# Optimization experiments

Hardware: AMD Instinct MI355X
Metric: run time of the kernel (lower is better)

Reference implementation:

```python
import jax, jax.numpy as jnp
import numpy as np

EPS = 1e-5

def setup_inputs() -> dict:
    key = jax.random.key(0)
    ks = jax.random.split(key, 8)
    B, T, D, S = 8, 4096, 1024, 64
    return {
        "x": jax.random.normal(ks[0], (B, T, D), dtype=jnp.float32),
        "time_decay": jax.random.normal(ks[1], (S,), dtype=jnp.float32) * 0.1 - 0.5,
        "time_first": jax.random.normal(ks[2], (S,), dtype=jnp.float32) * 0.1,
        "W_key": jax.random.normal(ks[3], (S, D), dtype=jnp.float32) * 0.02,
        "W_value": jax.random.normal(ks[4], (S, D), dtype=jnp.float32) * 0.02,
        "W_output": jax.random.normal(ks[5], (D, S), dtype=jnp.float32) * 0.02,
        "W_shift": jax.random.normal(ks[6], (D, D), dtype=jnp.float32) * 0.02,
        "shift_gate": jnp.ones((D,), dtype=jnp.float32),
        "ln_w": jnp.ones((D,), dtype=jnp.float32),
        "ln_b": jnp.zeros((D,), dtype=jnp.float32),
    }


def _forward(x, time_decay, time_first, W_key, W_value, W_output, W_shift, shift_gate, ln_w, ln_b):
    B, T, D = x.shape
    S = time_decay.shape[0]
    # --- token shift: rotate sequence by shift_len, project, gated blend ---
    shift_len = max(1, int(T * 0.5))
    x_cat = jnp.concatenate([x[:, shift_len:], x[:, :-shift_len]], axis=1)  # (B,T,D)
    gate = jax.nn.sigmoid(shift_gate)
    x_shift = jnp.einsum('btd,ed->bte', x_cat, W_shift) * gate + x * (1.0 - gate)
    # --- layernorm (torch: biased variance, eps=1e-5) ---
    mu = jnp.mean(x_shift, axis=-1, keepdims=True)
    var = jnp.mean(jnp.square(x_shift - mu), axis=-1, keepdims=True)
    xn = (x_shift - mu) * jax.lax.rsqrt(var + EPS) * ln_w + ln_b
    # --- key/value projections and per-step wkv (fully vectorized) ---
    k = jnp.einsum('btd,sd->bts', xn, W_key)    # (B,T,S)
    v = jnp.einsum('btd,sd->bts', xn, W_value)  # (B,T,S)
    wkv = jnp.exp(-jnp.exp(time_first) * jax.nn.sigmoid(k)) * v  # (B,T,S)
    # --- linear recurrence: state = state*w + wkv_t, scanned over T ---
    w = jnp.exp(time_decay)  # (S,)
    def step(state, wkv_t):
        state = state * w + wkv_t
        return state, state
    init = jnp.zeros((B, S), dtype=x.dtype)
    last_state, states = jax.lax.scan(step, init, jnp.swapaxes(wkv, 0, 1))  # states: (T,B,S)
    states = jnp.swapaxes(states, 0, 1)  # (B,T,S)
    # --- batched output projection (applied per-step in torch; same math) ---
    output = jnp.einsum('bts,ds->btd', states, W_output)  # (B,T,D)
    return output, last_state


def reference(x, time_decay, time_first, W_key, W_value, W_output, W_shift, shift_gate, ln_w, ln_b):
    out, last_state = _forward(x, time_decay, time_first, W_key, W_value, W_output, W_shift, shift_gate, ln_w, ln_b)
    return out, jax.lax.stop_gradient(last_state)
```

## Files before the change

### kernel.cpp

```cpp
#include <hip/hip_runtime.h>
#include <stdint.h>

#define B_ 8
#define T_ 4096
#define D_ 1024
#define S_ 64
#define N_ 32768
#define OUT_ELEMS 33554432
#define NCHK 128
#define CHKL 32

typedef __attribute__((ext_vector_type(8))) short bf16x8;
typedef __attribute__((ext_vector_type(8))) unsigned short u16x8;
typedef __attribute__((ext_vector_type(4))) float f32x4;

__device__ __forceinline__ uint16_t f2bf(float f) {
    union { float f; uint32_t u; } v; v.f = f;
    uint32_t r = v.u + 0x7FFFu + ((v.u >> 16) & 1u);
    return (uint16_t)(r >> 16);
}
__device__ __forceinline__ float bf2f(uint16_t h) {
    union { uint32_t u; float f; } v; v.u = ((uint32_t)h) << 16;
    return v.f;
}

#define GLOAD_LDS16(gp, lp)                                             \
    __builtin_amdgcn_global_load_lds(                                   \
        (const __attribute__((address_space(1))) void*)(gp),            \
        (__attribute__((address_space(3))) void*)(lp), 16, 0, 0)

__global__ void cast_f32_bf16(const float* __restrict__ src,
                              uint16_t* __restrict__ dst, int n4) {
    int i = blockIdx.x * blockDim.x + threadIdx.x;
    if (i >= n4) return;
    float4 v = ((const float4*)src)[i];
    ushort4 o;
    o.x = f2bf(v.x); o.y = f2bf(v.y); o.z = f2bf(v.z); o.w = f2bf(v.w);
    ((ushort4*)dst)[i] = o;
}

__global__ __launch_bounds__(256) void k1_shift_gemm(
    const uint16_t* __restrict__ xb, const uint16_t* __restrict__ Wsb,
    const float* __restrict__ shift_gate, uint16_t* __restrict__ xs)
{
    __shared__ uint16_t As[128][64];
    __shared__ uint16_t Bs[128][64];
    const int tid = threadIdx.x;
    const int w = tid >> 6, lane = tid & 63, quad = lane >> 4, l16 = lane & 15;
    const int wm = w >> 1, wn = w & 1;
    const int m0 = blockIdx.y * 128;
    const int n0 = blockIdx.x * 128;
    const int m0x = m0 ^ 2048;

    const int srow = w * 32 + (lane >> 3);
    const int scg  = ((lane & 7) ^ (lane >> 3)) * 8;
    const uint16_t* aG = xb  + (size_t)(m0x + srow) * D_ + scg;
    const uint16_t* bG = Wsb + (size_t)(n0  + srow) * D_ + scg;

    f32x4 acc[4][4];
#pragma unroll
    for (int i = 0; i < 4; ++i)
#pragma unroll
        for (int j = 0; j < 4; ++j) acc[i][j] = (f32x4){0.f, 0.f, 0.f, 0.f};

    for (int k0 = 0; k0 < D_; k0 += 64) {
        __syncthreads();
#pragma unroll
        for (int i = 0; i < 4; ++i) {
            GLOAD_LDS16(aG + k0 + (size_t)(i * 8) * D_, &As[w * 32 + i * 8][0]);
            GLOAD_LDS16(bG + k0 + (size_t)(i * 8) * D_, &Bs[w * 32 + i * 8][0]);
        }
        __syncthreads();
#pragma unroll
        for (int ks = 0; ks < 2; ++ks) {
            bf16x8 a[4], b[4];
#pragma unroll
            for (int i = 0; i < 4; ++i) {
                int ra = wm * 64 + i * 16 + l16;
                a[i] = *(const bf16x8*)&As[ra][(((ks * 4 + quad) ^ (l16 & 7)) * 8)];
            }
#pragma unroll
            for (int j = 0; j < 4; ++j) {
                int rb = wn * 64 + j * 16 + l16;
                b[j] = *(const bf16x8*)&Bs[rb][(((ks * 4 + quad) ^ (l16 & 7)) * 8)];
            }
#pragma unroll
            for (int i = 0; i < 4; ++i)
#pragma unroll
                for (int j = 0; j < 4; ++j)
                    acc[i][j] = __builtin_amdgcn_mfma_f32_16x16x32_bf16(
                        a[i], b[j], acc[i][j], 0, 0, 0);
        }
    }

#pragma unroll
    for (int j = 0; j < 4; ++j) {
        int col = n0 + wn * 64 + j * 16 + l16;
        float g = 1.f / (1.f + __expf(-shift_gate[col]));
        float omg = 1.f - g;
#pragma unroll
        for (int i = 0; i < 4; ++i) {
            int row = m0 + wm * 64 + i * 16 + quad * 4;
#pragma unroll
            for (int r = 0; r < 4; ++r) {
                float res = acc[i][j][r] * g +
                            bf2f(xb[(size_t)(row + r) * D_ + col]) * omg;
                xs[(size_t)(row + r) * D_ + col] = f2bf(res);
            }
        }
    }
}

__global__ __launch_bounds__(256) void k2_ln(uint16_t* __restrict__ xs,
                                             const float* __restrict__ ln_w,
                                             const float* __restrict__ ln_b)
{
    const int w = threadIdx.x >> 6, lane = threadIdx.x & 63;
    const size_t row = (size_t)blockIdx.x * 4 + w;
    uint16_t* p = xs + row * D_ + lane * 16;

    u16x8 h0 = *(const u16x8*)p;
    u16x8 h1 = *(const u16x8*)(p + 8);
    float v[16];
#pragma unroll
    for (int i = 0; i < 8; ++i) { v[i] = bf2f(h0[i]); v[8 + i] = bf2f(h1[i]); }
    float s = 0.f, q = 0.f;
#pragma unroll
    for (int i = 0; i < 16; ++i) { s += v[i]; q += v[i] * v[i]; }
#pragma unroll
    for (int off = 32; off > 0; off >>= 1) {
        s += __shfl_xor(s, off);
        q += __shfl_xor(q, off);
    }
    float mu = s * (1.f / D_);
    float var = q * (1.f / D_) - mu * mu;
    float rstd = rsqrtf(var + 1e-5f);

    const float* lw = ln_w + lane * 16;
    const float* lb = ln_b + lane * 16;
    u16x8 o0, o1;
#pragma unroll
    for (int i = 0; i < 8; ++i) {
        o0[i] = f2bf((v[i] - mu) * rstd * lw[i] + lb[i]);
        o1[i] = f2bf((v[8 + i] - mu) * rstd * lw[8 + i] + lb[8 + i]);
    }
    *(u16x8*)p = o0;
    *(u16x8*)(p + 8) = o1;
}

__global__ __launch_bounds__(256) void k3_kv(
    const uint16_t* __restrict__ xn, const uint16_t* __restrict__ Wkvb,
    const float* __restrict__ time_first, float* __restrict__ wkv)
{
    __shared__ float tile[2][128][65];
    const int tid = threadIdx.x;
    const int w = tid >> 6, lane = tid & 63, quad = lane >> 4, l16 = lane & 15;
    const int wm = w >> 1, wn = w & 1;
    const int bm0 = blockIdx.x * 128;
    const int m0 = bm0 + wm * 64;

    const uint16_t* aptr[4];
    const uint16_t* bptr[4];
#pragma unroll
    for (int i = 0; i < 4; ++i) {
        aptr[i] = xn + (size_t)(m0 + i * 16 + l16) * D_ + quad * 8;
        bptr[i] = Wkvb + (size_t)(wn * 64 + i * 16 + l16) * D_ + quad * 8;
    }

    f32x4 acc[4][4];
#pragma unroll
    for (int i = 0; i < 4; ++i)
#pragma unroll
        for (int j = 0; j < 4; ++j) acc[i][j] = (f32x4){0.f, 0.f, 0.f, 0.f};

    for (int k = 0; k < D_; k += 32) {
        bf16x8 a[4], b[4];
#pragma unroll
        for (int i = 0; i < 4; ++i) a[i] = *(const bf16x8*)(aptr[i] + k);
#pragma unroll
        for (int i = 0; i < 4; ++i) b[i] = *(const bf16x8*)(bptr[i] + k);
#pragma unroll
        for (int i = 0; i < 4; ++i)
#pragma unroll
            for (int j = 0; j < 4; ++j)
                acc[i][j] = __builtin_amdgcn_mfma_f32_16x16x32_bf16(
                    a[i], b[j], acc[i][j], 0, 0, 0);
    }

#pragma unroll
    for (int i = 0; i < 4; ++i)
#pragma unroll
        for (int j = 0; j < 4; ++j)
#pragma unroll
            for (int r = 0; r < 4; ++r) {
                int rl = wm * 64 + i * 16 + quad * 4 + r;
                int cl = j * 16 + l16;
                tile[wn][rl][cl] = acc[i][j][r];
            }
    __syncthreads();

    for (int e = tid; e < 128 * 64; e += 256) {
        int rl = e >> 6, s = e & 63;
        float kk = tile[0][rl][s];
        float vv = tile[1][rl][s];
        float sig = 1.f / (1.f + __expf(-kk));
        float res = __expf(-__expf(time_first[s]) * sig) * vv;
        wkv[(size_t)(bm0 + rl) * S_ + s] = res;
    }
}

__global__ void k4a(const float* __restrict__ wkv,
                    const float* __restrict__ time_decay,
                    float* __restrict__ part)
{
    const int s = threadIdx.x;
    const int bc = blockIdx.x;
    const int b = bc >> 7, c = bc & (NCHK - 1);
    float w = expf(time_decay[s]);
    const float* src = wkv + ((size_t)b * T_ + c * CHKL) * S_ + s;
    float st = 0.f;
    for (int t = 0; t < CHKL; ++t) st = st * w + src[(size_t)t * S_];
    part[(size_t)bc * S_ + s] = st;
}
__global__ void k4b(const float* __restrict__ part,
                    const float* __restrict__ time_decay,
                    float* __restrict__ carry)
{
    const int s = threadIdx.x;
    const int b = blockIdx.x;
    float wL = expf(time_decay[s] * (float)CHKL);
    float cin = 0.f;
    for (int c = 0; c < NCHK; ++c) {
        size_t idx = ((size_t)b * NCHK + c) * S_ + s;
        carry[idx] = cin;
        cin = cin * wL + part[idx];
    }
}
__global__ void k4c(const float* __restrict__ wkv,
                    const float* __restrict__ time_decay,
                    const float* __restrict__ carry,
                    uint16_t* __restrict__ stb,
                    float* __restrict__ last_state)
{
    const int s = threadIdx.x;
    const int bc = blockIdx.x;
    const int b = bc >> 7, c = bc & (NCHK - 1);
    float w = expf(time_decay[s]);
    const float* src = wkv + ((size_t)b * T_ + c * CHKL) * S_ + s;
    uint16_t* dst = stb + ((size_t)b * T_ + c * CHKL) * S_ + s;
    float st = carry[(size_t)bc * S_ + s];
    for (int t = 0; t < CHKL; ++t) {
        st = st * w + src[(size_t)t * S_];
        dst[(size_t)t * S_] = f2bf(st);
    }
    if (c == NCHK - 1) last_state[b * S_ + s] = st;
}

__global__ __launch_bounds__(256) void k5_out(
    const uint16_t* __restrict__ st, const uint16_t* __restrict__ Wob,
    float* __restrict__ out)
{
    const int tid = threadIdx.x;
    const int w = tid >> 6, lane = tid & 63, quad = lane >> 4, l16 = lane & 15;
    const int wm = w >> 1, wn = w & 1;
    const int m0 = blockIdx.y * 128 + wm * 64;
    const int n0 = blockIdx.x * 128 + wn * 64;

    f32x4 acc[4][4];
#pragma unroll
    for (int i = 0; i < 4; ++i)
#pragma unroll
        for (int j = 0; j < 4; ++j) acc[i][j] = (f32x4){0.f, 0.f, 0.f, 0.f};

#pragma unroll
    for (int k = 0; k < S_; k += 32) {
        bf16x8 a[4], b[4];
#pragma unroll
        for (int i = 0; i < 4; ++i)
            a[i] = *(const bf16x8*)(st + (size_t)(m0 + i * 16 + l16) * S_ + k + quad * 8);
#pragma unroll
        for (int i = 0; i < 4; ++i)
            b[i] = *(const bf16x8*)(Wob + (size_t)(n0 + i * 16 + l16) * S_ + k + quad * 8);
#pragma unroll
        for (int i = 0; i < 4; ++i)
#pragma unroll
            for (int j = 0; j < 4; ++j)
                acc[i][j] = __builtin_amdgcn_mfma_f32_16x16x32_bf16(
                    a[i], b[j], acc[i][j], 0, 0, 0);
    }

#pragma unroll
    for (int j = 0; j < 4; ++j) {
        int col = n0 + j * 16 + l16;
#pragma unroll
        for (int i = 0; i < 4; ++i) {
            int row = m0 + i * 16 + quad * 4;
#pragma unroll
            for (int r = 0; r < 4; ++r)
                out[(size_t)(row + r) * D_ + col] = acc[i][j][r];
        }
    }
}

extern "C" void kernel_launch(void* const* d_in, const int* in_sizes, int n_in,
                              void* d_out, int out_size, void* d_ws, size_t ws_size,
                              hipStream_t stream) {
    const float* x          = (const float*)d_in[0];
    const float* time_decay = (const float*)d_in[1];
    const float* time_first = (const float*)d_in[2];
    const float* W_key      = (const float*)d_in[3];
    const float* W_value    = (const float*)d_in[4];
    const float* W_output   = (const float*)d_in[5];
    const float* W_shift    = (const float*)d_in[6];
    const float* shift_gate = (const float*)d_in[7];
    const float* ln_w       = (const float*)d_in[8];
    const float* ln_b       = (const float*)d_in[9];
    float* out = (float*)d_out;

    char* ws = (char*)d_ws;
    uint16_t* xb   = (uint16_t*)(ws + 0);
    uint16_t* xs   = (uint16_t*)(ws + 67108864);
    float*    wkv  = (float*)   (ws + 134217728);
    uint16_t* stb  = (uint16_t*)(ws + 142606336);
    uint16_t* Wsb  = (uint16_t*)(ws + 146800640);
    uint16_t* Wkvb = (uint16_t*)(ws + 148897792);
    uint16_t* Wob  = (uint16_t*)(ws + 149159936);
    float*    part = (float*)   (ws + 149291008);
    float*    carry= (float*)   (ws + 149553152);

    cast_f32_bf16<<<32768, 256, 0, stream>>>(x, xb, OUT_ELEMS / 4);
    cast_f32_bf16<<<1024, 256, 0, stream>>>(W_shift, Wsb, (D_ * D_) / 4);
    cast_f32_bf16<<<64, 256, 0, stream>>>(W_key, Wkvb, (S_ * D_) / 4);
    cast_f32_bf16<<<64, 256, 0, stream>>>(W_value, Wkvb + S_ * D_, (S_ * D_) / 4);
    cast_f32_bf16<<<64, 256, 0, stream>>>(W_output, Wob, (D_ * S_) / 4);

    k1_shift_gemm<<<dim3(8, 256), 256, 0, stream>>>(xb, Wsb, shift_gate, xs);
    k2_ln<<<N_ / 4, 256, 0, stream>>>(xs, ln_w, ln_b);
    k3_kv<<<256, 256, 0, stream>>>(xs, Wkvb, time_first, wkv);
    k4a<<<B_ * NCHK, S_, 0, stream>>>(wkv, time_decay, part);
    k4b<<<B_, S_, 0, stream>>>(part, time_decay, carry);
    k4c<<<B_ * NCHK, S_, 0, stream>>>(wkv, time_decay, carry, stb, out + OUT_ELEMS);
    k5_out<<<dim3(8, 256), 256, 0, stream>>>(stb, Wob, out);
}
```

Before: 445.3 us.

## Merge weight casts, coalesce GEMM epilogues via LDS, tile k3 through LDS

The four small weight-cast launches become one prep kernel, which also precomputes the sigmoid of the shift gate and exp(time_first). The k1 and k5 epilogues are staged through shared memory so each thread writes wide, coalesced row segments instead of scattered scalar stores. k1 also gets a remapped 1D grid intended to improve L2 reuse. k3 now loads its tiles with async global-to-LDS copies into swizzled shared memory, uses 64-row tiles to double the block count, and runs a vectorised epilogue. The cost is extra LDS traffic and barriers in the epilogues.

```diff
diff --git a/kernel.cpp b/kernel.cpp
--- a/kernel.cpp
+++ b/kernel.cpp
@@ -39,21 +39,61 @@
     ((ushort4*)dst)[i] = o;
 }
 
+__global__ void wprep(const float* __restrict__ Wsf, const float* __restrict__ Wkf,
+                      const float* __restrict__ Wvf, const float* __restrict__ Wof,
+                      const float* __restrict__ sg, const float* __restrict__ tf,
+                      uint16_t* __restrict__ Wsb, uint16_t* __restrict__ Wkvb,
+                      uint16_t* __restrict__ Wob, float* __restrict__ gbuf,
+                      float* __restrict__ efirst)
+{
+    int i = blockIdx.x * blockDim.x + threadIdx.x;
+    const float* src; uint16_t* dst; int j;
+    if (i < 262144) { src = Wsf; dst = Wsb; j = i; }
+    else if (i < 278528) { src = Wkf; dst = Wkvb; j = i - 262144; }
+    else if (i < 294912) { src = Wvf; dst = Wkvb + 65536; j = i - 278528; }
+    else if (i < 311296) { src = Wof; dst = Wob; j = i - 294912; }
+    else if (i < 311552) {
+        j = i - 311296;
+        float4 v = ((const float4*)sg)[j];
+        float4 g;
+        g.x = 1.f / (1.f + __expf(-v.x)); g.y = 1.f / (1.f + __expf(-v.y));
+        g.z = 1.f / (1.f + __expf(-v.z)); g.w = 1.f / (1.f + __expf(-v.w));
+        ((float4*)gbuf)[j] = g;
+        return;
+    } else if (i < 311568) {
+        j = i - 311552;
+        float4 v = ((const float4*)tf)[j];
+        float4 e;
+        e.x = __expf(v.x); e.y = __expf(v.y); e.z = __expf(v.z); e.w = __expf(v.w);
+        ((float4*)efirst)[j] = e;
+        return;
+    } else return;
+    float4 v = ((const float4*)src)[j];
+    ushort4 o;
+    o.x = f2bf(v.x); o.y = f2bf(v.y); o.z = f2bf(v.z); o.w = f2bf(v.w);
+    ((ushort4*)dst)[j] = o;
+}
+
 __global__ __launch_bounds__(256) void k1_shift_gemm(
     const uint16_t* __restrict__ xb, const uint16_t* __restrict__ Wsb,
-    const float* __restrict__ shift_gate, uint16_t* __restrict__ xs)
-{
-    __shared__ uint16_t As[128][64];
-    __shared__ uint16_t Bs[128][64];
+    const float* __restrict__ gbuf, uint16_t* __restrict__ xs)
+{
+    __shared__ char sh[34816];
+    uint16_t (*As)[64] = (uint16_t(*)[64])sh;
+    uint16_t (*Bs)[64] = (uint16_t(*)[64])(sh + 16384);
+    float (*epi)[68] = (float(*)[68])sh;
+
     const int tid = threadIdx.x;
     const int w = tid >> 6, lane = tid & 63, quad = lane >> 4, l16 = lane & 15;
     const int wm = w >> 1, wn = w & 1;
-    const int m0 = blockIdx.y * 128;
-    const int n0 = blockIdx.x * 128;
+    const int lin = blockIdx.x;
+    const int mt = (lin & 7) * 32 + (lin >> 6);
+    const int nt = (lin >> 3) & 7;
+    const int m0 = mt * 128, n0 = nt * 128;
     const int m0x = m0 ^ 2048;
 
     const int srow = w * 32 + (lane >> 3);
-    const int scg  = ((lane & 7) ^ (lane >> 3)) * 8;
+    const int scg  = ((lane & 7) ^ ((lane >> 3) & 7)) * 8;
     const uint16_t* aG = xb  + (size_t)(m0x + srow) * D_ + scg;
     const uint16_t* bG = Wsb + (size_t)(n0  + srow) * D_ + scg;
 
@@ -75,15 +115,13 @@
         for (int ks = 0; ks < 2; ++ks) {
             bf16x8 a[4], b[4];
 #pragma unroll
-            for (int i = 0; i < 4; ++i) {
-                int ra = wm * 64 + i * 16 + l16;
-                a[i] = *(const bf16x8*)&As[ra][(((ks * 4 + quad) ^ (l16 & 7)) * 8)];
-            }
-#pragma unroll
-            for (int j = 0; j < 4; ++j) {
-                int rb = wn * 64 + j * 16 + l16;
-                b[j] = *(const bf16x8*)&Bs[rb][(((ks * 4 + quad) ^ (l16 & 7)) * 8)];
-            }
+            for (int i = 0; i < 4; ++i)
+                a[i] = *(const bf16x8*)&As[wm * 64 + i * 16 + l16]
+                                         [(((ks * 4 + quad) ^ (l16 & 7)) * 8)];
+#pragma unroll
+            for (int j = 0; j < 4; ++j)
+                b[j] = *(const bf16x8*)&Bs[wn * 64 + j * 16 + l16]
+                                         [(((ks * 4 + quad) ^ (l16 & 7)) * 8)];
 #pragma unroll
             for (int i = 0; i < 4; ++i)
 #pragma unroll
@@ -93,20 +131,36 @@
         }
     }
 
-#pragma unroll
-    for (int j = 0; j < 4; ++j) {
-        int col = n0 + wn * 64 + j * 16 + l16;
-        float g = 1.f / (1.f + __expf(-shift_gate[col]));
-        float omg = 1.f - g;
-#pragma unroll
-        for (int i = 0; i < 4; ++i) {
-            int row = m0 + wm * 64 + i * 16 + quad * 4;
-#pragma unroll
-            for (int r = 0; r < 4; ++r) {
-                float res = acc[i][j][r] * g +
-                            bf2f(xb[(size_t)(row + r) * D_ + col]) * omg;
-                xs[(size_t)(row + r) * D_ + col] = f2bf(res);
-            }
+    const int row = tid >> 1;
+    const int c0 = (tid & 1) * 32;
+#pragma unroll
+    for (int h = 0; h < 2; ++h) {
+        __syncthreads();
+        if (wn == h) {
+#pragma unroll
+            for (int i = 0; i < 4; ++i)
+#pragma unroll
+                for (int j = 0; j < 4; ++j)
+#pragma unroll
+                    for (int r = 0; r < 4; ++r)
+                        epi[wm * 64 + i * 16 + quad * 4 + r][j * 16 + l16] =
+                            acc[i][j][r];
+        }
+        __syncthreads();
+        const int col = n0 + h * 64 + c0;
+        const uint16_t* xrow = xb + (size_t)(m0 + row) * D_ + col;
+        uint16_t* orow = xs + (size_t)(m0 + row) * D_ + col;
+#pragma unroll
+        for (int c4 = 0; c4 < 8; ++c4) {
+            float4 g4 = ((const float4*)(gbuf + col))[c4];
+            ushort4 xh = ((const ushort4*)xrow)[c4];
+            const float* e = &epi[row][c0 + c4 * 4];
+            ushort4 o;
+            o.x = f2bf(e[0] * g4.x + bf2f(xh.x) * (1.f - g4.x));
+            o.y = f2bf(e[1] * g4.y + bf2f(xh.y) * (1.f - g4.y));
+            o.z = f2bf(e[2] * g4.z + bf2f(xh.z) * (1.f - g4.z));
+            o.w = f2bf(e[3] * g4.w + bf2f(xh.w) * (1.f - g4.w));
+            ((ushort4*)orow)[c4] = o;
         }
     }
 }
@@ -150,62 +204,82 @@
 
 __global__ __launch_bounds__(256) void k3_kv(
     const uint16_t* __restrict__ xn, const uint16_t* __restrict__ Wkvb,
-    const float* __restrict__ time_first, float* __restrict__ wkv)
-{
-    __shared__ float tile[2][128][65];
+    const float* __restrict__ efirst, float* __restrict__ wkv)
+{
+    __shared__ char sh[33792];
+    uint16_t (*As)[64] = (uint16_t(*)[64])sh;
+    uint16_t (*Bs)[64] = (uint16_t(*)[64])(sh + 8192);
+    float (*epi)[132] = (float(*)[132])sh;
+
     const int tid = threadIdx.x;
     const int w = tid >> 6, lane = tid & 63, quad = lane >> 4, l16 = lane & 15;
     const int wm = w >> 1, wn = w & 1;
-    const int bm0 = blockIdx.x * 128;
-    const int m0 = bm0 + wm * 64;
-
-    const uint16_t* aptr[4];
-    const uint16_t* bptr[4];
-#pragma unroll
-    for (int i = 0; i < 4; ++i) {
-        aptr[i] = xn + (size_t)(m0 + i * 16 + l16) * D_ + quad * 8;
-        bptr[i] = Wkvb + (size_t)(wn * 64 + i * 16 + l16) * D_ + quad * 8;
-    }
-
-    f32x4 acc[4][4];
-#pragma unroll
-    for (int i = 0; i < 4; ++i)
+    const int m0 = blockIdx.x * 64;
+
+    const int lrow = w * 8 + (lane >> 3);
+    const int scg  = ((lane & 7) ^ ((lane >> 3) & 7)) * 8;
+    const uint16_t* aG = xn + (size_t)(m0 + lrow) * D_ + scg;
+    const uint16_t* bG = Wkvb + (size_t)lrow * D_ + scg;
+
+    f32x4 acc[2][4];
+#pragma unroll
+    for (int i = 0; i < 2; ++i)
 #pragma unroll
         for (int j = 0; j < 4; ++j) acc[i][j] = (f32x4){0.f, 0.f, 0.f, 0.f};
 
-    for (int k = 0; k < D_; k += 32) {
-        bf16x8 a[4], b[4];
-#pragma unroll
-        for (int i = 0; i < 4; ++i) a[i] = *(const bf16x8*)(aptr[i] + k);
-#pragma unroll
-        for (int i = 0; i < 4; ++i) b[i] = *(const bf16x8*)(bptr[i] + k);
+    for (int k0 = 0; k0 < D_; k0 += 64) {
+        __syncthreads();
+#pragma unroll
+        for (int i = 0; i < 2; ++i)
+            GLOAD_LDS16(aG + k0 + (size_t)(i * 32) * D_, &As[lrow - (lane >> 3) + i * 32][0]);
 #pragma unroll
         for (int i = 0; i < 4; ++i)
+            GLOAD_LDS16(bG + k0 + (size_t)(i * 32) * D_, &Bs[lrow - (lane >> 3) + i * 32][0]);
+        __syncthreads();
+#pragma unroll
+        for (int ks = 0; ks < 2; ++ks) {
+            bf16x8 a[2], b[4];
+#pragma unroll
+            for (int i = 0; i < 2; ++i)
+                a[i] = *(const bf16x8*)&As[wm * 32 + i * 16 + l16]
+                                         [(((ks * 4 + quad) ^ (l16 & 7)) * 8)];
 #pragma unroll
             for (int j = 0; j < 4; ++j)
-                acc[i][j] = __builtin_amdgcn_mfma_f32_16x16x32_bf16(
-                    a[i], b[j], acc[i][j], 0, 0, 0);
-    }
-
-#pragma unroll
-    for (int i = 0; i < 4; ++i)
+                b[j] = *(const bf16x8*)&Bs[wn * 64 + j * 16 + l16]
+                                         [(((ks * 4 + quad) ^ (l16 & 7)) * 8)];
+#pragma unroll
+            for (int i = 0; i < 2; ++i)
+#pragma unroll
+                for (int j = 0; j < 4; ++j)
+                    acc[i][j] = __builtin_amdgcn_mfma_f32_16x16x32_bf16(
+                        a[i], b[j], acc[i][j], 0, 0, 0);
+        }
+    }
+
+    __syncthreads();
+#pragma unroll
+    for (int i = 0; i < 2; ++i)
 #pragma unroll
         for (int j = 0; j < 4; ++j)
 #pragma unroll
-            for (int r = 0; r < 4; ++r) {
-                int rl = wm * 64 + i * 16 + quad * 4 + r;
-                int cl = j * 16 + l16;
-                tile[wn][rl][cl] = acc[i][j][r];
-            }
+            for (int r = 0; r < 4; ++r)
+                epi[wm * 32 + i * 16 + quad * 4 + r][wn * 64 + j * 16 + l16] =
+                    acc[i][j][r];
     __syncthreads();
 
-    for (int e = tid; e < 128 * 64; e += 256) {
-        int rl = e >> 6, s = e & 63;
-        float kk = tile[0][rl][s];
-        float vv = tile[1][rl][s];
-        float sig = 1.f / (1.f + __expf(-kk));
-        float res = __expf(-__expf(time_first[s]) * sig) * vv;
-        wkv[(size_t)(bm0 + rl) * S_ + s] = res;
+    const int row = tid >> 2, s0 = (tid & 3) * 16;
+    float* dst = wkv + (size_t)(m0 + row) * S_ + s0;
+#pragma unroll
+    for (int c4 = 0; c4 < 4; ++c4) {
+        float4 kk = *(const float4*)&epi[row][s0 + c4 * 4];
+        float4 vv = *(const float4*)&epi[row][64 + s0 + c4 * 4];
+        float4 ef = ((const float4*)(efirst + s0))[c4];
+        float4 o;
+        o.x = __expf(-ef.x / (1.f + __expf(-kk.x))) * vv.x;
+        o.y = __expf(-ef.y / (1.f + __expf(-kk.y))) * vv.y;
+        o.z = __expf(-ef.z / (1.f + __expf(-kk.z))) * vv.z;
+        o.w = __expf(-ef.w / (1.f + __expf(-kk.w))) * vv.w;
+        *(float4*)(dst + c4 * 4) = o;
     }
 }
 
@@ -260,11 +334,12 @@
     const uint16_t* __restrict__ st, const uint16_t* __restrict__ Wob,
     float* __restrict__ out)
 {
+    __shared__ float epi[128][68];
     const int tid = threadIdx.x;
     const int w = tid >> 6, lane = tid & 63, quad = lane >> 4, l16 = lane & 15;
     const int wm = w >> 1, wn = w & 1;
-    const int m0 = blockIdx.y * 128 + wm * 64;
-    const int n0 = blockIdx.x * 128 + wn * 64;
+    const int m0b = blockIdx.y * 128;
+    const int n0b = blockIdx.x * 128;
 
     f32x4 acc[4][4];
 #pragma unroll
@@ -277,10 +352,10 @@
         bf16x8 a[4], b[4];
 #pragma unroll
         for (int i = 0; i < 4; ++i)
-            a[i] = *(const bf16x8*)(st + (size_t)(m0 + i * 16 + l16) * S_ + k + quad * 8);
+            a[i] = *(const bf16x8*)(st + (size_t)(m0b + wm * 64 + i * 16 + l16) * S_ + k + quad * 8);
 #pragma unroll
         for (int i = 0; i < 4; ++i)
-            b[i] = *(const bf16x8*)(Wob + (size_t)(n0 + i * 16 + l16) * S_ + k + quad * 8);
+            b[i] = *(const bf16x8*)(Wob + (size_t)(n0b + wn * 64 + i * 16 + l16) * S_ + k + quad * 8);
 #pragma unroll
         for (int i = 0; i < 4; ++i)
 #pragma unroll
@@ -289,16 +364,26 @@
                     a[i], b[j], acc[i][j], 0, 0, 0);
     }
 
-#pragma unroll
-    for (int j = 0; j < 4; ++j) {
-        int col = n0 + j * 16 + l16;
-#pragma unroll
-        for (int i = 0; i < 4; ++i) {
-            int row = m0 + i * 16 + quad * 4;
-#pragma unroll
-            for (int r = 0; r < 4; ++r)
-                out[(size_t)(row + r) * D_ + col] = acc[i][j][r];
-        }
+    const int row = tid >> 1;
+    const int c0 = (tid & 1) * 32;
+#pragma unroll
+    for (int h = 0; h < 2; ++h) {
+        __syncthreads();
+        if (wn == h) {
+#pragma unroll
+            for (int i = 0; i < 4; ++i)
+#pragma unroll
+                for (int j = 0; j < 4; ++j)
+#pragma unroll
+                    for (int r = 0; r < 4; ++r)
+                        epi[wm * 64 + i * 16 + quad * 4 + r][j * 16 + l16] =
+                            acc[i][j][r];
+        }
+        __syncthreads();
+        float* dst = out + (size_t)(m0b + row) * D_ + n0b + h * 64 + c0;
+#pragma unroll
+        for (int c4 = 0; c4 < 8; ++c4)
+            ((float4*)dst)[c4] = *(const float4*)&epi[row][c0 + c4 * 4];
     }
 }
 
@@ -318,25 +403,26 @@
     float* out = (float*)d_out;
 
     char* ws = (char*)d_ws;
-    uint16_t* xb   = (uint16_t*)(ws + 0);
-    uint16_t* xs   = (uint16_t*)(ws + 67108864);
-    float*    wkv  = (float*)   (ws + 134217728);
-    uint16_t* stb  = (uint16_t*)(ws + 142606336);
-    uint16_t* Wsb  = (uint16_t*)(ws + 146800640);
-    uint16_t* Wkvb = (uint16_t*)(ws + 148897792);
-    uint16_t* Wob  = (uint16_t*)(ws + 149159936);
-    float*    part = (float*)   (ws + 149291008);
-    float*    carry= (float*)   (ws + 149553152);
+    uint16_t* xb    = (uint16_t*)(ws + 0);
+    uint16_t* xs    = (uint16_t*)(ws + 67108864);
+    float*    wkv   = (float*)   (ws + 134217728);
+    uint16_t* stb   = (uint16_t*)(ws + 142606336);
+    uint16_t* Wsb   = (uint16_t*)(ws + 146800640);
+    uint16_t* Wkvb  = (uint16_t*)(ws + 148897792);
+    uint16_t* Wob   = (uint16_t*)(ws + 149159936);
+    float*    part  = (float*)   (ws + 149291008);
+    float*    carry = (float*)   (ws + 149553152);
+    float*    gbuf  = (float*)   (ws + 149815296);
+    float*    efirst= (float*)   (ws + 149819392);
 
     cast_f32_bf16<<<32768, 256, 0, stream>>>(x, xb, OUT_ELEMS / 4);
-    cast_f32_bf16<<<1024, 256, 0, stream>>>(W_shift, Wsb, (D_ * D_) / 4);
-    cast_f32_bf16<<<64, 256, 0, stream>>>(W_key, Wkvb, (S_ * D_) / 4);
-    cast_f32_bf16<<<64, 256, 0, stream>>>(W_value, Wkvb + S_ * D_, (S_ * D_) / 4);
-    cast_f32_bf16<<<64, 256, 0, stream>>>(W_output, Wob, (D_ * S_) / 4);
-
-    k1_shift_gemm<<<dim3(8, 256), 256, 0, stream>>>(xb, Wsb, shift_gate, xs);
+    wprep<<<1218, 256, 0, stream>>>(W_shift, W_key, W_value, W_output,
+                                    shift_gate, time_first,
+                                    Wsb, Wkvb, Wob, gbuf, efirst);
+
+    k1_shift_gemm<<<2048, 256, 0, stream>>>(xb, Wsb, gbuf, xs);
     k2_ln<<<N_ / 4, 256, 0, stream>>>(xs, ln_w, ln_b);
-    k3_kv<<<256, 256, 0, stream>>>(xs, Wkvb, time_first, wkv);
+    k3_kv<<<512, 256, 0, stream>>>(xs, Wkvb, efirst, wkv);
     k4a<<<B_ * NCHK, S_, 0, stream>>>(wkv, time_decay, part);
     k4b<<<B_, S_, 0, stream>>>(part, time_decay, carry);
     k4c<<<B_ * NCHK, S_, 0, stream>>>(wkv, time_decay, carry, stb, out + OUT_ELEMS);
```

Result: faster. 430.9 us (-3.2%).
